# Kernel optimization log

Measured on AMD Instinct MI355X. Metric: run time of the kernel, lower is better.

Reference implementation:

```python
import jax, jax.numpy as jnp
import numpy as np

D = 64       # hidden_dim
ED = 16      # edge_dim
N = 50000
E = 400000
T = 2
STEP = 0.5   # euler fixed step over t in [0,1] -> 2 steps
EPS = 1e-5

def setup_inputs() -> dict:
    key = jax.random.key(0)
    ks = jax.random.split(key, 14)
    def lin(k, fi, fo):
        return jax.random.normal(k, (fi, fo), jnp.float32) / np.sqrt(fi)
    return {
        'h_seq': jax.random.normal(ks[0], (T, N, D), jnp.float32),
        'edge_attr': jax.random.normal(ks[1], (T, E, ED), jnp.float32),
        # msg_net: MLP(2D+ED -> D -> D), 2 layers with ReLU
        'W1': lin(ks[2], 2 * D + ED, D), 'b1': jnp.zeros((D,), jnp.float32),
        'W2': lin(ks[3], D, D),          'b2': jnp.zeros((D,), jnp.float32),
        # dynamics_net: Linear(2D,D) -> LayerNorm -> SiLU -> Linear(D,D) -> Tanh
        'Wd1': lin(ks[4], 2 * D, D), 'bd1': jnp.zeros((D,), jnp.float32),
        'ln_g': jnp.ones((D,), jnp.float32), 'ln_b': jnp.zeros((D,), jnp.float32),
        'Wd2': lin(ks[5], D, D), 'bd2': jnp.zeros((D,), jnp.float32),
        'edge_index': jax.random.randint(ks[6], (T, 2, E), 0, N, jnp.int32),
    }

def _ode_func(h, row, col, ea, W1, b1, W2, b2, Wd1, bd1, ln_g, ln_b, Wd2, bd2):
    # identity transport: Q_uv @ h_v == h_v
    h_transported = h[col]                              # [E, D]
    msg_in = jnp.concatenate([h[row], h_transported, ea], axis=-1)  # [E, 2D+ED]
    msg = jax.nn.relu(msg_in @ W1 + b1) @ W2 + b2       # [E, D]
    agg = jax.ops.segment_sum(msg, row, num_segments=h.shape[0])    # [N, D]
    x = jnp.concatenate([h, agg], axis=-1) @ Wd1 + bd1  # [N, D]
    mu = x.mean(-1, keepdims=True)
    var = x.var(-1, keepdims=True)
    x = (x - mu) * jax.lax.rsqrt(var + EPS) * ln_g + ln_b
    x = jax.nn.silu(x) @ Wd2 + bd2
    return jnp.tanh(x)

def reference(h_seq, edge_attr, W1, b1, W2, b2, Wd1, bd1, ln_g, ln_b, Wd2, bd2, edge_index):
    params = (W1, b1, W2, b2, Wd1, bd1, ln_g, ln_b, Wd2, bd2)
    n_steps = int(round(1.0 / STEP))
    h_prev = h_seq[0]
    disagreements = []
    for t in range(T):
        row, col = edge_index[t, 0], edge_index[t, 1]
        ea = edge_attr[t]
        h = h_prev + h_seq[t]                           # h_fused
        for _ in range(n_steps):                        # fixed-step Euler
            h = h + STEP * _ode_func(h, row, col, ea, *params)
        diff = h[row] - h[col]                          # Q=I -> h_u - h_v
        disagreements.append(jnp.minimum((diff * diff).sum(-1), 1e4))
        h_prev = h
    return h_prev, jnp.stack(disagreements)             # h_final [N,D], D [T,E]
```

## Files before the change

### kernel.cpp

```cpp
#include <hip/hip_runtime.h>

#define NN 50000
#define EE 400000
#define NT64 6250
#define EGRID 1250
#define NBLK 782
#define SBLK 49

typedef __bf16 bf16x8 __attribute__((ext_vector_type(8)));
typedef float f32x4 __attribute__((ext_vector_type(4)));

static __device__ __forceinline__ ushort f2bf(float f) {
    union { float f; unsigned int i; } x; x.f = f;
    unsigned int r = x.i + 0x7fffu + ((x.i >> 16) & 1u);
    return (ushort)(r >> 16);
}
static __device__ __forceinline__ float bf2f(ushort u) {
    union { unsigned int i; float f; } x; x.i = ((unsigned int)u) << 16; return x.f;
}
static __device__ __forceinline__ unsigned pack2(float lo, float hi) {
    return (unsigned)f2bf(lo) | ((unsigned)f2bf(hi) << 16);
}
static __device__ __forceinline__ float fast_tanh(float x) {
    float e = __expf(2.f * x);
    return 1.f - 2.f / (e + 1.f);
}
static __device__ __forceinline__ bf16x8 pk8(float4 f0, float4 f1) {
    union { uint4 u; bf16x8 v; } z;
    z.u = make_uint4(pack2(f0.x, f0.y), pack2(f0.z, f0.w),
                     pack2(f1.x, f1.y), pack2(f1.z, f1.w));
    return z.v;
}
static __device__ __forceinline__ bf16x8 zero8() {
    union { uint4 u; bf16x8 v; } z;
    z.u = make_uint4(0u, 0u, 0u, 0u);
    return z.v;
}

__global__ __launch_bounds__(256) void prep_edge_k(
    const float* __restrict__ W1, const float* __restrict__ W2,
    const float* __restrict__ b1, const float* __restrict__ b2,
    ushort* __restrict__ B1P, ushort* __restrict__ B2P,
    float* __restrict__ b1f, float* __restrict__ b2f)
{
    int idx = blockIdx.x * 256 + threadIdx.x;
    if (idx < 10240) {
        int j = idx & 7, n = (idx >> 3) & 63, qk = idx >> 9;
        int kc = qk >> 2, quad = qk & 3;
        int k = kc * 32 + quad * 8 + j;
        B1P[idx] = (k < 144) ? f2bf(W1[k * 64 + n]) : (ushort)0;
    }
    if (idx < 4096) {
        int j = idx & 7, n = (idx >> 3) & 63, qk = idx >> 9;
        int kc = qk >> 2, quad = qk & 3;
        int k = kc * 32 + quad * 8 + j;
        B2P[idx] = f2bf(W2[k * 64 + n]);
    }
    if (idx < 64) { b1f[idx] = b1[idx]; b2f[idx] = b2[idx]; }
}

__global__ __launch_bounds__(256) void prep_node_k(
    const float* __restrict__ Wd1, const float* __restrict__ Wd2,
    const float* __restrict__ bd1, const float* __restrict__ lng,
    const float* __restrict__ lnb, const float* __restrict__ bd2,
    ushort* __restrict__ Wd1P, ushort* __restrict__ Wd2P,
    float* __restrict__ bd1f, float* __restrict__ lngf,
    float* __restrict__ lnbf, float* __restrict__ bd2f)
{
    int idx = blockIdx.x * 256 + threadIdx.x;
    if (idx < 8192) {
        int j = idx & 7, n = (idx >> 3) & 63, qk = idx >> 9;
        int kc = qk >> 2, quad = qk & 3;
        int k = kc * 32 + quad * 8 + j;
        Wd1P[idx] = f2bf(Wd1[k * 64 + n]);
    }
    if (idx < 4096) {
        int j = idx & 7, n = (idx >> 3) & 63, qk = idx >> 9;
        int kc = qk >> 2, quad = qk & 3;
        int k = kc * 32 + quad * 8 + j;
        Wd2P[idx] = f2bf(Wd2[k * 64 + n]);
    }
    if (idx < 64) {
        bd1f[idx] = bd1[idx]; lngf[idx] = lng[idx];
        lnbf[idx] = lnb[idx]; bd2f[idx] = bd2[idx];
    }
}

__global__ __launch_bounds__(256) void state_k(
    float* __restrict__ h, ushort* __restrict__ hb,
    const float* __restrict__ hseq_t, int mode)
{
    int i = blockIdx.x * 256 + threadIdx.x;
    float v = hseq_t[i];
    float r = (mode == 0) ? (2.f * v) : (h[i] + v);
    h[i] = r; hb[i] = f2bf(r);
}

__global__ __launch_bounds__(256) void zero_k(int* __restrict__ p, int n) {
    int i = blockIdx.x * 256 + threadIdx.x;
    if (i < n) p[i] = 0;
}
__global__ __launch_bounds__(256) void zero_f(float* __restrict__ p) {
    int i = blockIdx.x * 256 + threadIdx.x;
    p[i] = 0.f;
}
__global__ __launch_bounds__(256) void hist_k(const int* __restrict__ rows, int* __restrict__ counts) {
    int e = blockIdx.x * 256 + threadIdx.x;
    if (e < EE) atomicAdd(&counts[rows[e]], 1);
}

__global__ __launch_bounds__(256) void scanA_k(
    const int* __restrict__ counts, int* __restrict__ offsets, int* __restrict__ bsum)
{
    __shared__ int wsum[4];
    int tid = threadIdx.x, lane = tid & 63, w = tid >> 6;
    int i4 = blockIdx.x * 1024 + tid * 4;
    int4 v = make_int4(0, 0, 0, 0);
    if (i4 + 3 < NN) v = *(const int4*)(counts + i4);
    else {
        if (i4 < NN) v.x = counts[i4];
        if (i4 + 1 < NN) v.y = counts[i4 + 1];
        if (i4 + 2 < NN) v.z = counts[i4 + 2];
    }
    int s = v.x + v.y + v.z + v.w;
    int x = s;
    for (int off = 1; off < 64; off <<= 1) {
        int y = __shfl_up(x, off);
        if (lane >= off) x += y;
    }
    if (lane == 63) wsum[w] = x;
    __syncthreads();
    int wpre = 0;
    for (int j = 0; j < w; j++) wpre += wsum[j];
    int excl = wpre + x - s;
    int e0 = excl, e1 = e0 + v.x, e2 = e1 + v.y, e3 = e2 + v.z;
    if (i4 + 3 < NN) *(int4*)(offsets + i4) = make_int4(e0, e1, e2, e3);
    else {
        if (i4 < NN) offsets[i4] = e0;
        if (i4 + 1 < NN) offsets[i4 + 1] = e1;
        if (i4 + 2 < NN) offsets[i4 + 2] = e2;
    }
    if (tid == 255) bsum[blockIdx.x] = wpre + x;
}
__global__ __launch_bounds__(256) void scanC_k(
    int* __restrict__ offsets, const int* __restrict__ bsum, int* __restrict__ cursor)
{
    int i = blockIdx.x * 256 + threadIdx.x;
    if (i < NN) {
        int b = i >> 10;
        int add = 0;
        for (int j = 0; j < b; j++) add += bsum[j];
        int o = offsets[i] + add;
        offsets[i] = o; cursor[i] = o;
    }
    if (i == 0) offsets[NN] = EE;
}

__global__ __launch_bounds__(256) void fill_idx_k(
    const int* __restrict__ rows, int* __restrict__ cursor, int* __restrict__ esort)
{
    int e = blockIdx.x * 256 + threadIdx.x;
    if (e < EE) {
        int p = atomicAdd(&cursor[rows[e]], 1);
        if ((unsigned)p < (unsigned)EE) esort[p] = e;
    }
}

__global__ __launch_bounds__(256) void gather_k(
    const int* __restrict__ esort, const int* __restrict__ rows,
    const int* __restrict__ cols, const float* __restrict__ ea,
    int* __restrict__ rsort, int* __restrict__ csort, ushort* __restrict__ eab)
{
    int p = blockIdx.x * 256 + threadIdx.x;
    if (p < EE) {
        int e = esort[p];
        rsort[p] = rows[e];
        csort[p] = cols[e];
        const float* sp = ea + (size_t)e * 16;
        float4 f0 = ((const float4*)sp)[0], f1 = ((const float4*)sp)[1];
        float4 f2 = ((const float4*)sp)[2], f3 = ((const float4*)sp)[3];
        uint4* dp = (uint4*)(eab + (size_t)p * 16);
        dp[0] = make_uint4(pack2(f0.x, f0.y), pack2(f0.z, f0.w),
                           pack2(f1.x, f1.y), pack2(f1.z, f1.w));
        dp[1] = make_uint4(pack2(f2.x, f2.y), pack2(f2.z, f2.w),
                           pack2(f3.x, f3.y), pack2(f3.z, f3.w));
    }
}

__global__ __launch_bounds__(256, 5) void edge_k(
    const ushort* __restrict__ hb,
    const int* __restrict__ ridx, const int* __restrict__ cidx,
    const ushort* __restrict__ eab,
    const ushort* __restrict__ B1P, const ushort* __restrict__ B2P,
    const float* __restrict__ b1f, const float* __restrict__ b2f,
    ushort* __restrict__ msg)
{
    __shared__ __attribute__((aligned(16))) ushort sB1[10240];
    __shared__ __attribute__((aligned(16))) ushort sH[64 * 72];

    int tid = threadIdx.x;
    int lane = tid & 63, wave = tid >> 6;
    int m = lane & 15, quad = lane >> 4;

    for (int i = tid; i < 10240 / 8; i += 256) ((uint4*)sB1)[i] = ((const uint4*)B1P)[i];
    bf16x8 b2r[2][4];
    for (int kc = 0; kc < 2; kc++)
        for (int nt = 0; nt < 4; nt++)
            b2r[kc][nt] = *(const bf16x8*)(B2P + ((kc * 4 + quad) * 64 + nt * 16 + m) * 8);
    float b1v[4], b2v[4];
    for (int nt = 0; nt < 4; nt++) { b1v[nt] = b1f[nt * 16 + m]; b2v[nt] = b2f[nt * 16 + m]; }
    __syncthreads();

    ushort* sHw = sH + wave * 1152;
    int sl = wave * 16 + m;
    int t0 = blockIdx.x * 5;
    int r_n = ridx[t0 * 64 + sl], c_n = cidx[t0 * 64 + sl];

    for (int t = t0; t < t0 + 5; t++) {
        int s = t * 64 + sl;
        int r = r_n, c = c_n;

        bf16x8 a[5];
        a[0] = *(const bf16x8*)(hb + (size_t)r * 64 + quad * 8);
        a[1] = *(const bf16x8*)(hb + (size_t)r * 64 + 32 + quad * 8);
        a[2] = *(const bf16x8*)(hb + (size_t)c * 64 + quad * 8);
        a[3] = *(const bf16x8*)(hb + (size_t)c * 64 + 32 + quad * 8);
        a[4] = zero8();
        if (quad < 2) a[4] = *(const bf16x8*)(eab + (size_t)s * 16 + quad * 8);

        int tn = t + 1; if (tn >= t0 + 5) tn = t;
        int sn = tn * 64 + sl;
        r_n = ridx[sn]; c_n = cidx[sn];

        f32x4 acc[4];
        #pragma unroll
        for (int nt = 0; nt < 4; nt++) acc[nt] = (f32x4){0.f, 0.f, 0.f, 0.f};
        #pragma unroll
        for (int kc = 0; kc < 5; kc++) {
            #pragma unroll
            for (int nt = 0; nt < 4; nt++) {
                bf16x8 b = *(const bf16x8*)(sB1 + ((kc * 4 + quad) * 64 + nt * 16 + m) * 8);
                acc[nt] = __builtin_amdgcn_mfma_f32_16x16x32_bf16(a[kc], b, acc[nt], 0, 0, 0);
            }
        }

        __builtin_amdgcn_wave_barrier();
        #pragma unroll
        for (int nt = 0; nt < 4; nt++) {
            int colid = nt * 16 + m;
            float bb = b1v[nt];
            #pragma unroll
            for (int rr = 0; rr < 4; rr++) {
                float v = acc[nt][rr] + bb;
                v = v > 0.f ? v : 0.f;
                sHw[(quad * 4 + rr) * 72 + colid] = f2bf(v);
            }
        }
        __builtin_amdgcn_wave_barrier();

        f32x4 acc2[4];
        #pragma unroll
        for (int nt = 0; nt < 4; nt++) acc2[nt] = (f32x4){0.f, 0.f, 0.f, 0.f};
        #pragma unroll
        for (int kc = 0; kc < 2; kc++) {
            bf16x8 av = *(const bf16x8*)(sHw + m * 72 + kc * 32 + quad * 8);
            #pragma unroll
            for (int nt = 0; nt < 4; nt++) {
                acc2[nt] = __builtin_amdgcn_mfma_f32_16x16x32_bf16(av, b2r[kc][nt], acc2[nt], 0, 0, 0);
            }
        }

        #pragma unroll
        for (int nt = 0; nt < 4; nt++) {
            int colid = nt * 16 + m;
            float bb = b2v[nt];
            #pragma unroll
            for (int rr = 0; rr < 4; rr++) {
                int so = t * 64 + wave * 16 + quad * 4 + rr;
                msg[(size_t)so * 64 + colid] = f2bf(acc2[nt][rr] + bb);
            }
        }
    }
}

__global__ __launch_bounds__(256, 5) void nodeagg_k(
    float* __restrict__ h, ushort* __restrict__ hbm,
    const ushort* __restrict__ msg, const int* __restrict__ offsets,
    const ushort* __restrict__ Wd1P, const ushort* __restrict__ Wd2P,
    const float* __restrict__ bd1f, const float* __restrict__ lngf,
    const float* __restrict__ lnbf, const float* __restrict__ bd2f)
{
    __shared__ __attribute__((aligned(16))) float aggL[64][68];
    __shared__ __attribute__((aligned(16))) ushort sX[64 * 72];
    int tid = threadIdx.x;
    int lane = tid & 63, wave = tid >> 6;
    int m = lane & 15, quad = lane >> 4;
    int nbase = blockIdx.x * 64;

    for (int idx = wave; idx < 64; idx += 4) {
        int n = nbase + idx;
        float a = 0.f;
        if (n < NN) {
            int bgn = offsets[n], end2 = offsets[n + 1];
            int i = bgn;
            for (; i + 4 <= end2; i += 4) {
                a += bf2f(msg[(size_t)i * 64 + lane]);
                a += bf2f(msg[(size_t)(i + 1) * 64 + lane]);
                a += bf2f(msg[(size_t)(i + 2) * 64 + lane]);
                a += bf2f(msg[(size_t)(i + 3) * 64 + lane]);
            }
            for (; i < end2; i++) a += bf2f(msg[(size_t)i * 64 + lane]);
        }
        aggL[idx][lane] = a;
    }

    float gA[4], bA[4], d1[4], d2[4];
    for (int nt = 0; nt < 4; nt++) {
        int f = nt * 16 + m;
        d1[nt] = bd1f[f]; gA[nt] = lngf[f]; bA[nt] = lnbf[f]; d2[nt] = bd2f[f];
    }
    __syncthreads();

    int n_true = nbase + wave * 16 + m;
    bool own = (n_true < NN);
    int n = own ? n_true : (NN - 1);
    int nl = wave * 16 + m;
    bf16x8 A[4];
    A[0] = *(const bf16x8*)(hbm + (size_t)n * 64 + quad * 8);
    A[1] = *(const bf16x8*)(hbm + (size_t)n * 64 + 32 + quad * 8);
    {
        float4 g0 = *(const float4*)&aggL[nl][quad * 8];
        float4 g1 = *(const float4*)&aggL[nl][quad * 8 + 4];
        float4 g2 = *(const float4*)&aggL[nl][32 + quad * 8];
        float4 g3 = *(const float4*)&aggL[nl][32 + quad * 8 + 4];
        A[2] = pk8(g0, g1);
        A[3] = pk8(g2, g3);
    }

    f32x4 acc[4];
    #pragma unroll
    for (int nt = 0; nt < 4; nt++) acc[nt] = (f32x4){0.f, 0.f, 0.f, 0.f};
    #pragma unroll
    for (int kc = 0; kc < 4; kc++) {
        #pragma unroll
        for (int nt = 0; nt < 4; nt++) {
            bf16x8 b = *(const bf16x8*)(Wd1P + ((kc * 4 + quad) * 64 + nt * 16 + m) * 8);
            acc[nt] = __builtin_amdgcn_mfma_f32_16x16x32_bf16(A[kc], b, acc[nt], 0, 0, 0);
        }
    }

    float xs[4][4];
    #pragma unroll
    for (int nt = 0; nt < 4; nt++)
        #pragma unroll
        for (int r = 0; r < 4; r++)
            xs[nt][r] = acc[nt][r] + d1[nt];

    ushort* sXw = sX + wave * 1152;
    #pragma unroll
    for (int r = 0; r < 4; r++) {
        float s1 = 0.f, s2 = 0.f;
        #pragma unroll
        for (int nt = 0; nt < 4; nt++) { float v = xs[nt][r]; s1 += v; s2 += v * v; }
        for (int off = 1; off < 16; off <<= 1) {
            s1 += __shfl_xor(s1, off);
            s2 += __shfl_xor(s2, off);
        }
        float mean = s1 * (1.f / 64.f);
        float var = fmaxf(s2 * (1.f / 64.f) - mean * mean, 0.f);
        float rstd = rsqrtf(var + 1e-5f);
        #pragma unroll
        for (int nt = 0; nt < 4; nt++) {
            float xn = (xs[nt][r] - mean) * rstd * gA[nt] + bA[nt];
            float slv = xn / (1.f + __expf(-xn));
            sXw[(quad * 4 + r) * 72 + nt * 16 + m] = f2bf(slv);
        }
    }
    __builtin_amdgcn_wave_barrier();

    f32x4 acc2[4];
    #pragma unroll
    for (int nt = 0; nt < 4; nt++) acc2[nt] = (f32x4){0.f, 0.f, 0.f, 0.f};
    #pragma unroll
    for (int kc = 0; kc < 2; kc++) {
        bf16x8 av = *(const bf16x8*)(sXw + m * 72 + kc * 32 + quad * 8);
        #pragma unroll
        for (int nt = 0; nt < 4; nt++) {
            bf16x8 b = *(const bf16x8*)(Wd2P + ((kc * 4 + quad) * 64 + nt * 16 + m) * 8);
            acc2[nt] = __builtin_amdgcn_mfma_f32_16x16x32_bf16(av, b, acc2[nt], 0, 0, 0);
        }
    }

    #pragma unroll
    for (int r = 0; r < 4; r++) {
        int g = nbase + wave * 16 + quad * 4 + r;
        if (g < NN) {
            #pragma unroll
            for (int nt = 0; nt < 4; nt++) {
                int f = nt * 16 + m;
                float y = fast_tanh(acc2[nt][r] + d2[nt]);
                float hn = h[(size_t)g * 64 + f] + 0.5f * y;
                h[(size_t)g * 64 + f] = hn;
                hbm[(size_t)g * 64 + f] = f2bf(hn);
            }
        }
    }
}

__global__ __launch_bounds__(256, 5) void edge_fb_k(
    const ushort* __restrict__ hb,
    const int* __restrict__ ridx, const int* __restrict__ cidx,
    const float* __restrict__ eaf,
    const ushort* __restrict__ B1P, const ushort* __restrict__ B2P,
    const float* __restrict__ b1f, const float* __restrict__ b2f,
    float* __restrict__ agg)
{
    __shared__ __attribute__((aligned(16))) ushort sB1[10240];
    __shared__ __attribute__((aligned(16))) ushort sH[64 * 72];

    int tid = threadIdx.x;
    int lane = tid & 63, wave = tid >> 6;
    int m = lane & 15, quad = lane >> 4;

    for (int i = tid; i < 10240 / 8; i += 256) ((uint4*)sB1)[i] = ((const uint4*)B1P)[i];
    bf16x8 b2r[2][4];
    for (int kc = 0; kc < 2; kc++)
        for (int nt = 0; nt < 4; nt++)
            b2r[kc][nt] = *(const bf16x8*)(B2P + ((kc * 4 + quad) * 64 + nt * 16 + m) * 8);
    float b1v[4], b2v[4];
    for (int nt = 0; nt < 4; nt++) { b1v[nt] = b1f[nt * 16 + m]; b2v[nt] = b2f[nt * 16 + m]; }
    __syncthreads();

    ushort* sHw = sH + wave * 1152;
    int sl = wave * 16 + m;
    int t0 = blockIdx.x * 5;

    for (int t = t0; t < t0 + 5; t++) {
        int s = t * 64 + sl;
        int r = ridx[s], c = cidx[s];
        bf16x8 a[5];
        a[0] = *(const bf16x8*)(hb + (size_t)r * 64 + quad * 8);
        a[1] = *(const bf16x8*)(hb + (size_t)r * 64 + 32 + quad * 8);
        a[2] = *(const bf16x8*)(hb + (size_t)c * 64 + quad * 8);
        a[3] = *(const bf16x8*)(hb + (size_t)c * 64 + 32 + quad * 8);
        a[4] = zero8();
        if (quad < 2) {
            const float* sp = eaf + (size_t)s * 16 + quad * 8;
            a[4] = pk8(((const float4*)sp)[0], ((const float4*)sp)[1]);
        }
        f32x4 acc[4];
        #pragma unroll
        for (int nt = 0; nt < 4; nt++) acc[nt] = (f32x4){0.f, 0.f, 0.f, 0.f};
        #pragma unroll
        for (int kc = 0; kc < 5; kc++)
            #pragma unroll
            for (int nt = 0; nt < 4; nt++) {
                bf16x8 b = *(const bf16x8*)(sB1 + ((kc * 4 + quad) * 64 + nt * 16 + m) * 8);
                acc[nt] = __builtin_amdgcn_mfma_f32_16x16x32_bf16(a[kc], b, acc[nt], 0, 0, 0);
            }
        __builtin_amdgcn_wave_barrier();
        #pragma unroll
        for (int nt = 0; nt < 4; nt++) {
            float bb = b1v[nt];
            #pragma unroll
            for (int rr = 0; rr < 4; rr++) {
                float v = acc[nt][rr] + bb;
                v = v > 0.f ? v : 0.f;
                sHw[(quad * 4 + rr) * 72 + nt * 16 + m] = f2bf(v);
            }
        }
        __builtin_amdgcn_wave_barrier();
        f32x4 acc2[4];
        #pragma unroll
        for (int nt = 0; nt < 4; nt++) acc2[nt] = (f32x4){0.f, 0.f, 0.f, 0.f};
        #pragma unroll
        for (int kc = 0; kc < 2; kc++) {
            bf16x8 av = *(const bf16x8*)(sHw + m * 72 + kc * 32 + quad * 8);
            #pragma unroll
            for (int nt = 0; nt < 4; nt++)
                acc2[nt] = __builtin_amdgcn_mfma_f32_16x16x32_bf16(av, b2r[kc][nt], acc2[nt], 0, 0, 0);
        }
        int base = t * 64 + wave * 16 + quad * 4;
        int r0 = ridx[base], r1 = ridx[base + 1], r2 = ridx[base + 2], r3 = ridx[base + 3];
        #pragma unroll
        for (int nt = 0; nt < 4; nt++) {
            int colid = nt * 16 + m;
            float bb = b2v[nt];
            float v0 = acc2[nt][0] + bb, v1 = acc2[nt][1] + bb;
            float v2 = acc2[nt][2] + bb, v3 = acc2[nt][3] + bb;
            float sum = v0; int pr = r0;
            if (r1 == pr) sum += v1;
            else { atomicAdd(&agg[(size_t)pr * 64 + colid], sum); pr = r1; sum = v1; }
            if (r2 == pr) sum += v2;
            else { atomicAdd(&agg[(size_t)pr * 64 + colid], sum); pr = r2; sum = v2; }
            if (r3 == pr) sum += v3;
            else { atomicAdd(&agg[(size_t)pr * 64 + colid], sum); pr = r3; sum = v3; }
            atomicAdd(&agg[(size_t)pr * 64 + colid], sum);
        }
    }
}

__global__ __launch_bounds__(256, 4) void node_k(
    float* __restrict__ h, ushort* __restrict__ hbm,
    float* __restrict__ agg,
    const ushort* __restrict__ Wd1P, const ushort* __restrict__ Wd2P,
    const float* __restrict__ bd1f, const float* __restrict__ lngf,
    const float* __restrict__ lnbf, const float* __restrict__ bd2f)
{
    __shared__ __attribute__((aligned(16))) ushort sB1[8192];
    __shared__ __attribute__((aligned(16))) ushort sB2[4096];
    __shared__ __attribute__((aligned(16))) ushort sX[64 * 72];
    int tid = threadIdx.x;
    int lane = tid & 63, wave = tid >> 6;
    int m = lane & 15, quad = lane >> 4;
    int nbase = blockIdx.x * 64;

    for (int i = tid; i < 8192 / 8; i += 256) ((uint4*)sB1)[i] = ((const uint4*)Wd1P)[i];
    for (int i = tid; i < 4096 / 8; i += 256) ((uint4*)sB2)[i] = ((const uint4*)Wd2P)[i];
    float gA[4], bA[4], d1[4], d2[4];
    for (int nt = 0; nt < 4; nt++) {
        int f = nt * 16 + m;
        d1[nt] = bd1f[f]; gA[nt] = lngf[f]; bA[nt] = lnbf[f]; d2[nt] = bd2f[f];
    }
    __syncthreads();

    int n_true = nbase + wave * 16 + m;
    bool own = (n_true < NN);
    int n = own ? n_true : (NN - 1);
    bf16x8 A[4];
    A[0] = *(const bf16x8*)(hbm + (size_t)n * 64 + quad * 8);
    A[1] = *(const bf16x8*)(hbm + (size_t)n * 64 + 32 + quad * 8);
    {
        const float* ap = agg + (size_t)n * 64 + quad * 8;
        float4 g0 = ((const float4*)ap)[0], g1 = ((const float4*)ap)[1];
        const float* ap2 = agg + (size_t)n * 64 + 32 + quad * 8;
        float4 g2 = ((const float4*)ap2)[0], g3 = ((const float4*)ap2)[1];
        A[2] = pk8(g0, g1);
        A[3] = pk8(g2, g3);
        if (own) {
            float4 z = make_float4(0.f, 0.f, 0.f, 0.f);
            ((float4*)(agg + (size_t)n * 64 + quad * 8))[0] = z;
            ((float4*)(agg + (size_t)n * 64 + quad * 8))[1] = z;
            ((float4*)(agg + (size_t)n * 64 + 32 + quad * 8))[0] = z;
            ((float4*)(agg + (size_t)n * 64 + 32 + quad * 8))[1] = z;
        }
    }

    f32x4 acc[4];
    #pragma unroll
    for (int nt = 0; nt < 4; nt++) acc[nt] = (f32x4){0.f, 0.f, 0.f, 0.f};
    #pragma unroll
    for (int kc = 0; kc < 4; kc++)
        #pragma unroll
        for (int nt = 0; nt < 4; nt++) {
            bf16x8 b = *(const bf16x8*)(sB1 + ((kc * 4 + quad) * 64 + nt * 16 + m) * 8);
            acc[nt] = __builtin_amdgcn_mfma_f32_16x16x32_bf16(A[kc], b, acc[nt], 0, 0, 0);
        }

    float xs[4][4];
    #pragma unroll
    for (int nt = 0; nt < 4; nt++)
        #pragma unroll
        for (int r = 0; r < 4; r++)
            xs[nt][r] = acc[nt][r] + d1[nt];

    ushort* sXw = sX + wave * 1152;
    #pragma unroll
    for (int r = 0; r < 4; r++) {
        float s1 = 0.f, s2 = 0.f;
        #pragma unroll
        for (int nt = 0; nt < 4; nt++) { float v = xs[nt][r]; s1 += v; s2 += v * v; }
        for (int off = 1; off < 16; off <<= 1) {
            s1 += __shfl_xor(s1, off);
            s2 += __shfl_xor(s2, off);
        }
        float mean = s1 * (1.f / 64.f);
        float var = fmaxf(s2 * (1.f / 64.f) - mean * mean, 0.f);
        float rstd = rsqrtf(var + 1e-5f);
        #pragma unroll
        for (int nt = 0; nt < 4; nt++) {
            float xn = (xs[nt][r] - mean) * rstd * gA[nt] + bA[nt];
            float slv = xn / (1.f + __expf(-xn));
            sXw[(quad * 4 + r) * 72 + nt * 16 + m] = f2bf(slv);
        }
    }
    __builtin_amdgcn_wave_barrier();

    f32x4 acc2[4];
    #pragma unroll
    for (int nt = 0; nt < 4; nt++) acc2[nt] = (f32x4){0.f, 0.f, 0.f, 0.f};
    #pragma unroll
    for (int kc = 0; kc < 2; kc++) {
        bf16x8 av = *(const bf16x8*)(sXw + m * 72 + kc * 32 + quad * 8);
        #pragma unroll
        for (int nt = 0; nt < 4; nt++) {
            bf16x8 b = *(const bf16x8*)(sB2 + ((kc * 4 + quad) * 64 + nt * 16 + m) * 8);
            acc2[nt] = __builtin_amdgcn_mfma_f32_16x16x32_bf16(av, b, acc2[nt], 0, 0, 0);
        }
    }

    #pragma unroll
    for (int r = 0; r < 4; r++) {
        int g = nbase + wave * 16 + quad * 4 + r;
        if (g < NN) {
            #pragma unroll
            for (int nt = 0; nt < 4; nt++) {
                int f = nt * 16 + m;
                float y = fast_tanh(acc2[nt][r] + d2[nt]);
                float hn = h[(size_t)g * 64 + f] + 0.5f * y;
                h[(size_t)g * 64 + f] = hn;
                hbm[(size_t)g * 64 + f] = f2bf(hn);
            }
        }
    }
}

__global__ __launch_bounds__(256) void dis_k(
    const float* __restrict__ h, const int* __restrict__ rows,
    const int* __restrict__ cols, float* __restrict__ outp)
{
    int tid = threadIdx.x;
    int e = blockIdx.x * 16 + (tid >> 4);
    int l16 = tid & 15;
    int r = rows[e], c = cols[e];
    float4 a = *(const float4*)(h + (size_t)r * 64 + l16 * 4);
    float4 b = *(const float4*)(h + (size_t)c * 64 + l16 * 4);
    float dx = a.x - b.x, dy = a.y - b.y, dz = a.z - b.z, dw = a.w - b.w;
    float s = dx * dx + dy * dy + dz * dz + dw * dw;
    for (int off = 1; off < 16; off <<= 1) s += __shfl_xor(s, off);
    if (l16 == 0) outp[e] = (s < 1e4f ? s : 1e4f);
}

__global__ __launch_bounds__(256) void final_k(const float* __restrict__ h, float* __restrict__ out) {
    int i = blockIdx.x * 256 + threadIdx.x;
    out[i] = h[i];
}

extern "C" void kernel_launch(void* const* d_in, const int* in_sizes, int n_in,
                              void* d_out, int out_size, void* d_ws, size_t ws_size,
                              hipStream_t stream) {
    const float* h_seq = (const float*)d_in[0];
    const float* eattr = (const float*)d_in[1];
    const float* W1 = (const float*)d_in[2];
    const float* b1 = (const float*)d_in[3];
    const float* W2 = (const float*)d_in[4];
    const float* b2 = (const float*)d_in[5];
    const float* Wd1 = (const float*)d_in[6];
    const float* bd1 = (const float*)d_in[7];
    const float* lng = (const float*)d_in[8];
    const float* lnb = (const float*)d_in[9];
    const float* Wd2 = (const float*)d_in[10];
    const float* bd2 = (const float*)d_in[11];
    const int* ei = (const int*)d_in[12];
    float* out = (float*)d_out;

    char* wsp = (char*)d_ws;
    size_t used = 0;
    auto carve = [&](size_t b) {
        void* p = (void*)(wsp + used);
        used += (b + 255) & ~(size_t)255;
        return p;
    };
    float* h0     = (float*)carve((size_t)NN * 64 * 4);
    ushort* hb0   = (ushort*)carve((size_t)NN * 64 * 2);
    float* agg    = (float*)carve((size_t)NN * 64 * 4);
    ushort* B1P   = (ushort*)carve(10240 * 2);
    ushort* B2P   = (ushort*)carve(4096 * 2);
    ushort* Wd1P  = (ushort*)carve(8192 * 2);
    ushort* Wd2P  = (ushort*)carve(4096 * 2);
    float* b1f    = (float*)carve(256);
    float* b2f    = (float*)carve(256);
    float* bd1f   = (float*)carve(256);
    float* lngf   = (float*)carve(256);
    float* lnbf   = (float*)carve(256);
    float* bd2f   = (float*)carve(256);
    int* counts   = (int*)carve((size_t)NN * 4);
    int* offsets  = (int*)carve((size_t)(NN + 1) * 4);
    int* cursor   = (int*)carve((size_t)NN * 4);
    int* bsum     = (int*)carve(256);
    int* esort    = (int*)carve((size_t)EE * 4);
    int* rsort    = (int*)carve((size_t)EE * 4);
    int* csort    = (int*)carve((size_t)EE * 4);
    ushort* eab   = (ushort*)carve((size_t)EE * 16 * 2);
    ushort* msg   = (ushort*)carve((size_t)EE * 64 * 2);
    const bool full = (used <= ws_size);

    prep_edge_k<<<40, 256, 0, stream>>>(W1, W2, b1, b2, B1P, B2P, b1f, b2f);
    prep_node_k<<<32, 256, 0, stream>>>(Wd1, Wd2, bd1, lng, lnb, bd2, Wd1P, Wd2P, bd1f, lngf, lnbf, bd2f);
    if (!full) zero_f<<<12500, 256, 0, stream>>>(agg);

    for (int t = 0; t < 2; t++) {
        const int* rows = ei + (size_t)t * 2 * EE;
        const int* cols = rows + EE;
        const float* eat = eattr + (size_t)t * EE * 16;
        state_k<<<12500, 256, 0, stream>>>(h0, hb0, h_seq + (size_t)t * NN * 64, t);
        if (full) {
            zero_k<<<196, 256, 0, stream>>>(counts, NN);
            hist_k<<<1563, 256, 0, stream>>>(rows, counts);
            scanA_k<<<SBLK, 256, 0, stream>>>(counts, offsets, bsum);
            scanC_k<<<196, 256, 0, stream>>>(offsets, bsum, cursor);
            fill_idx_k<<<1563, 256, 0, stream>>>(rows, cursor, esort);
            gather_k<<<1563, 256, 0, stream>>>(esort, rows, cols, eat, rsort, csort, eab);
            for (int s = 0; s < 2; s++) {
                edge_k<<<EGRID, 256, 0, stream>>>(hb0, rsort, csort, eab,
                                                  B1P, B2P, b1f, b2f, msg);
                nodeagg_k<<<NBLK, 256, 0, stream>>>(h0, hb0, msg, offsets, Wd1P, Wd2P,
                                                    bd1f, lngf, lnbf, bd2f);
            }
        } else {
            for (int s = 0; s < 2; s++) {
                edge_fb_k<<<EGRID, 256, 0, stream>>>(hb0, rows, cols, eat,
                                                     B1P, B2P, b1f, b2f, agg);
                node_k<<<NBLK, 256, 0, stream>>>(h0, hb0, agg, Wd1P, Wd2P,
                                                 bd1f, lngf, lnbf, bd2f);
            }
        }
        dis_k<<<25000, 256, 0, stream>>>(h0, rows, cols, out + (size_t)NN * 64 + (size_t)t * EE);
    }
    final_k<<<12500, 256, 0, stream>>>(h0, out);
}
```

Measured before the change: 564.0 us.

## Batch CSR construction across both timesteps and software-pipeline edge gathers

The histogram, scan and fill kernels for both timesteps now run once up front, with a second grid dimension and per-timestep buffers, halving the launch count for sorting. In edge_k, the gathered h rows and edge attributes for the next tile are loaded into registers while the current tile's MFMAs run, and indices are prefetched two tiles ahead. The goal is to hide gather latency and cut launch overhead. The cost is more VGPRs, which may lower occupancy, and larger workspace buffers.

```diff
diff --git a/kernel.cpp b/kernel.cpp
--- a/kernel.cpp
+++ b/kernel.cpp
@@ -104,14 +104,18 @@
     int i = blockIdx.x * 256 + threadIdx.x;
     p[i] = 0.f;
 }
-__global__ __launch_bounds__(256) void hist_k(const int* __restrict__ rows, int* __restrict__ counts) {
+__global__ __launch_bounds__(256) void hist_k(const int* __restrict__ ei, int* __restrict__ counts) {
     int e = blockIdx.x * 256 + threadIdx.x;
-    if (e < EE) atomicAdd(&counts[rows[e]], 1);
-}
-
+    const int* rows = ei + (size_t)blockIdx.y * 2 * EE;
+    int* cnt = counts + blockIdx.y * NN;
+    if (e < EE) atomicAdd(&cnt[rows[e]], 1);
+}
 __global__ __launch_bounds__(256) void scanA_k(
-    const int* __restrict__ counts, int* __restrict__ offsets, int* __restrict__ bsum)
-{
+    const int* __restrict__ counts_, int* __restrict__ offsets_, int* __restrict__ bsum_)
+{
+    const int* counts = counts_ + blockIdx.y * NN;
+    int* offsets = offsets_ + blockIdx.y * (NN + 1);
+    int* bsum = bsum_ + blockIdx.y * 64;
     __shared__ int wsum[4];
     int tid = threadIdx.x, lane = tid & 63, w = tid >> 6;
     int i4 = blockIdx.x * 1024 + tid * 4;
@@ -143,8 +147,11 @@
     if (tid == 255) bsum[blockIdx.x] = wpre + x;
 }
 __global__ __launch_bounds__(256) void scanC_k(
-    int* __restrict__ offsets, const int* __restrict__ bsum, int* __restrict__ cursor)
-{
+    int* __restrict__ offsets_, const int* __restrict__ bsum_, int* __restrict__ cursor_)
+{
+    int* offsets = offsets_ + blockIdx.y * (NN + 1);
+    const int* bsum = bsum_ + blockIdx.y * 64;
+    int* cursor = cursor_ + blockIdx.y * NN;
     int i = blockIdx.x * 256 + threadIdx.x;
     if (i < NN) {
         int b = i >> 10;
@@ -155,11 +162,13 @@
     }
     if (i == 0) offsets[NN] = EE;
 }
-
 __global__ __launch_bounds__(256) void fill_idx_k(
-    const int* __restrict__ rows, int* __restrict__ cursor, int* __restrict__ esort)
+    const int* __restrict__ ei, int* __restrict__ cursor_, int* __restrict__ esort_)
 {
     int e = blockIdx.x * 256 + threadIdx.x;
+    const int* rows = ei + (size_t)blockIdx.y * 2 * EE;
+    int* cursor = cursor_ + blockIdx.y * NN;
+    int* esort = esort_ + (size_t)blockIdx.y * EE;
     if (e < EE) {
         int p = atomicAdd(&cursor[rows[e]], 1);
         if ((unsigned)p < (unsigned)EE) esort[p] = e;
@@ -214,23 +223,28 @@
     ushort* sHw = sH + wave * 1152;
     int sl = wave * 16 + m;
     int t0 = blockIdx.x * 5;
-    int r_n = ridx[t0 * 64 + sl], c_n = cidx[t0 * 64 + sl];
+
+    int rc = ridx[t0 * 64 + sl], cc = cidx[t0 * 64 + sl];
+    bf16x8 aC[5];
+    aC[0] = *(const bf16x8*)(hb + (size_t)rc * 64 + quad * 8);
+    aC[1] = *(const bf16x8*)(hb + (size_t)rc * 64 + 32 + quad * 8);
+    aC[2] = *(const bf16x8*)(hb + (size_t)cc * 64 + quad * 8);
+    aC[3] = *(const bf16x8*)(hb + (size_t)cc * 64 + 32 + quad * 8);
+    aC[4] = zero8();
+    if (quad < 2) aC[4] = *(const bf16x8*)(eab + (size_t)(t0 * 64 + sl) * 16 + quad * 8);
+    int rn = ridx[(t0 + 1) * 64 + sl], cn = cidx[(t0 + 1) * 64 + sl];
 
     for (int t = t0; t < t0 + 5; t++) {
-        int s = t * 64 + sl;
-        int r = r_n, c = c_n;
-
-        bf16x8 a[5];
-        a[0] = *(const bf16x8*)(hb + (size_t)r * 64 + quad * 8);
-        a[1] = *(const bf16x8*)(hb + (size_t)r * 64 + 32 + quad * 8);
-        a[2] = *(const bf16x8*)(hb + (size_t)c * 64 + quad * 8);
-        a[3] = *(const bf16x8*)(hb + (size_t)c * 64 + 32 + quad * 8);
-        a[4] = zero8();
-        if (quad < 2) a[4] = *(const bf16x8*)(eab + (size_t)s * 16 + quad * 8);
-
-        int tn = t + 1; if (tn >= t0 + 5) tn = t;
-        int sn = tn * 64 + sl;
-        r_n = ridx[sn]; c_n = cidx[sn];
+        int tn = (t + 1 < t0 + 5) ? t + 1 : t;
+        bf16x8 aN[5];
+        aN[0] = *(const bf16x8*)(hb + (size_t)rn * 64 + quad * 8);
+        aN[1] = *(const bf16x8*)(hb + (size_t)rn * 64 + 32 + quad * 8);
+        aN[2] = *(const bf16x8*)(hb + (size_t)cn * 64 + quad * 8);
+        aN[3] = *(const bf16x8*)(hb + (size_t)cn * 64 + 32 + quad * 8);
+        aN[4] = zero8();
+        if (quad < 2) aN[4] = *(const bf16x8*)(eab + (size_t)(tn * 64 + sl) * 16 + quad * 8);
+        int tnn = (t + 2 < t0 + 5) ? t + 2 : t;
+        int rn2 = ridx[tnn * 64 + sl], cn2 = cidx[tnn * 64 + sl];
 
         f32x4 acc[4];
         #pragma unroll
@@ -240,7 +254,7 @@
             #pragma unroll
             for (int nt = 0; nt < 4; nt++) {
                 bf16x8 b = *(const bf16x8*)(sB1 + ((kc * 4 + quad) * 64 + nt * 16 + m) * 8);
-                acc[nt] = __builtin_amdgcn_mfma_f32_16x16x32_bf16(a[kc], b, acc[nt], 0, 0, 0);
+                acc[nt] = __builtin_amdgcn_mfma_f32_16x16x32_bf16(aC[kc], b, acc[nt], 0, 0, 0);
             }
         }
 
@@ -280,6 +294,10 @@
                 msg[(size_t)so * 64 + colid] = f2bf(acc2[nt][rr] + bb);
             }
         }
+
+        #pragma unroll
+        for (int k2 = 0; k2 < 5; k2++) aC[k2] = aN[k2];
+        rn = rn2; cn = cn2;
     }
 }
 
@@ -674,11 +692,11 @@
     float* lngf   = (float*)carve(256);
     float* lnbf   = (float*)carve(256);
     float* bd2f   = (float*)carve(256);
-    int* counts   = (int*)carve((size_t)NN * 4);
-    int* offsets  = (int*)carve((size_t)(NN + 1) * 4);
-    int* cursor   = (int*)carve((size_t)NN * 4);
-    int* bsum     = (int*)carve(256);
-    int* esort    = (int*)carve((size_t)EE * 4);
+    int* counts   = (int*)carve((size_t)2 * NN * 4);
+    int* offsets  = (int*)carve((size_t)2 * (NN + 1) * 4);
+    int* cursor   = (int*)carve((size_t)2 * NN * 4);
+    int* bsum     = (int*)carve(512);
+    int* esort    = (int*)carve((size_t)2 * EE * 4);
     int* rsort    = (int*)carve((size_t)EE * 4);
     int* csort    = (int*)carve((size_t)EE * 4);
     ushort* eab   = (ushort*)carve((size_t)EE * 16 * 2);
@@ -688,6 +706,14 @@
     prep_edge_k<<<40, 256, 0, stream>>>(W1, W2, b1, b2, B1P, B2P, b1f, b2f);
     prep_node_k<<<32, 256, 0, stream>>>(Wd1, Wd2, bd1, lng, lnb, bd2, Wd1P, Wd2P, bd1f, lngf, lnbf, bd2f);
     if (!full) zero_f<<<12500, 256, 0, stream>>>(agg);
+
+    if (full) {
+        zero_k<<<391, 256, 0, stream>>>(counts, 2 * NN);
+        hist_k<<<dim3(1563, 2), 256, 0, stream>>>(ei, counts);
+        scanA_k<<<dim3(SBLK, 2), 256, 0, stream>>>(counts, offsets, bsum);
+        scanC_k<<<dim3(196, 2), 256, 0, stream>>>(offsets, bsum, cursor);
+        fill_idx_k<<<dim3(1563, 2), 256, 0, stream>>>(ei, cursor, esort);
+    }
 
     for (int t = 0; t < 2; t++) {
         const int* rows = ei + (size_t)t * 2 * EE;
@@ -695,16 +721,13 @@
         const float* eat = eattr + (size_t)t * EE * 16;
         state_k<<<12500, 256, 0, stream>>>(h0, hb0, h_seq + (size_t)t * NN * 64, t);
         if (full) {
-            zero_k<<<196, 256, 0, stream>>>(counts, NN);
-            hist_k<<<1563, 256, 0, stream>>>(rows, counts);
-            scanA_k<<<SBLK, 256, 0, stream>>>(counts, offsets, bsum);
-            scanC_k<<<196, 256, 0, stream>>>(offsets, bsum, cursor);
-            fill_idx_k<<<1563, 256, 0, stream>>>(rows, cursor, esort);
-            gather_k<<<1563, 256, 0, stream>>>(esort, rows, cols, eat, rsort, csort, eab);
+            gather_k<<<1563, 256, 0, stream>>>(esort + (size_t)t * EE, rows, cols, eat,
+                                               rsort, csort, eab);
+            const int* offs_t = offsets + (size_t)t * (NN + 1);
             for (int s = 0; s < 2; s++) {
                 edge_k<<<EGRID, 256, 0, stream>>>(hb0, rsort, csort, eab,
                                                   B1P, B2P, b1f, b2f, msg);
-                nodeagg_k<<<NBLK, 256, 0, stream>>>(h0, hb0, msg, offsets, Wd1P, Wd2P,
+                nodeagg_k<<<NBLK, 256, 0, stream>>>(h0, hb0, msg, offs_t, Wd1P, Wd2P,
                                                     bd1f, lngf, lnbf, bd2f);
             }
         } else {
```

After: 614.1 us. +8.9%, slower.
